# Kernel tuning notes

Measured on AMD Instinct MI355X. Metric: run time of the kernel, lower is better.

The kernel has to match this reference:

```python
import jax, jax.numpy as jnp
import numpy as np

K = 3            # kernel size (odd)
CO, CI = 16, 16  # out/in channels

def setup_inputs() -> dict:
    key = jax.random.key(0)
    k1, k2, k3, k4 = jax.random.split(key, 4)
    B, C, H, W = 4, CI, 128, 128
    input_data = jax.random.normal(k1, (B, C, H, W), dtype=jnp.float32)
    # fixation coordinates in pixel units
    foa_xy = jax.random.uniform(k2, (B, 2), dtype=jnp.float32) * jnp.array([W, H], jnp.float32)
    hidden = 256
    W1 = jax.random.normal(k3, (2, hidden), dtype=jnp.float32) * (1.0 / jnp.sqrt(2.0))
    b1 = jnp.zeros((hidden,), jnp.float32)
    W2 = jax.random.normal(k4, (hidden, CO * CI * K * K), dtype=jnp.float32) * (1.0 / jnp.sqrt(hidden))
    b2 = jnp.zeros((CO * CI * K * K,), jnp.float32)
    return {"input_data": input_data, "foa_xy": foa_xy, "W1": W1, "b1": b1, "W2": W2, "b2": b2}

def _unfold_reflect(x, k):
    # x: [B, C, H, W] -> patches [B, C, k*k, H*W], reflect padding, stride 1, dilation 1
    B, C, H, W = x.shape
    pad = (k - 1) // 2
    xp = jnp.pad(x, ((0, 0), (0, 0), (pad, pad), (pad, pad)), mode="reflect")
    rows = [xp[:, :, i:i + H, j:j + W] for i in range(k) for j in range(k)]
    return jnp.stack(rows, axis=2).reshape(B, C, k * k, H * W)

def reference(input_data, foa_xy, W1, b1, W2, b2):
    B, C, H, W = input_data.shape
    # coordinate grid [H*W, 2] as (x, y), matching torch meshgrid(ij) + stack(xx, yy)
    ys = jnp.arange(H, dtype=jnp.float32)
    xs = jnp.arange(W, dtype=jnp.float32)
    yy, xx = jnp.meshgrid(ys, xs, indexing="ij")
    coords = jnp.stack([xx.ravel(), yy.ravel()], axis=1)         # [HW, 2]
    net_in = (coords[None, :, :] - foa_xy[:, None, :]).reshape(B * H * W, 2)
    # kernel-generating MLP
    h = jax.nn.relu(net_in @ W1 + b1)
    net_out = h @ W2 + b2                                        # [B*HW, CO*CI*K*K]
    kernel = net_out.reshape(B, H * W, CO, CI, K * K)            # [B, P, o, i, q]
    patches = _unfold_reflect(input_data, K)                     # [B, CI, K*K, HW]
    # per-pixel conv: sum over in-channels and kernel taps
    out = jnp.einsum("biqp,bpoiq->bop", patches, kernel)         # [B, CO, HW]
    return out.reshape(B, CO, H, W)
```

## Files before the change

kernel.cpp:

```cpp
#include <hip/hip_runtime.h>

#define CI    16
#define CO    16
#define HID   256
#define KPAD  288
#define NKK   9
#define NKH   8
#define NCH   144
#define IMGH  128
#define IMGW  128
#define PTS   68
#define KKSTR (NCH * 32)
#define OSTRS (NKK * NCH * 32)

typedef float f32x4  __attribute__((ext_vector_type(4)));
typedef float f32x2  __attribute__((ext_vector_type(2)));
typedef short bf16x8 __attribute__((ext_vector_type(8)));

__device__ __host__ __forceinline__ short f2bf(float f) {
  union { float f; unsigned u; } c; c.f = f;
  unsigned b = c.u + 0x7FFFu + ((c.u >> 16) & 1u);
  return (short)(b >> 16);
}

__global__ void prep_w2(const float* __restrict__ W2, const float* __restrict__ b2,
                        short* __restrict__ W2b) {
  __shared__ float tile[32][65];
  const int kk = blockIdx.x % NKK;
  const int colbase = (blockIdx.x / NKK) * 64;
  const int tid = threadIdx.x;

  for (int e = tid; e < 2048; e += 256) {
    int klr = e >> 6;
    int cc  = e & 63;
    int col = colbase + cc;
    float v;
    if (kk < 8) v = W2[(kk * 32 + klr) * (CO * NCH) + col];
    else        v = (klr == 0) ? b2[col] : 0.f;
    tile[klr][cc] = v;
  }
  __syncthreads();
  for (int e = tid; e < 2048; e += 256) {
    int cc = e >> 5;
    int kl = e & 31;
    int col = colbase + cc;
    int o = col / NCH;
    int n = col - o * NCH;
    W2b[(((o * NKK + kk) * NCH + n) << 5) + kl] = f2bf(tile[kl][cc]);
  }
}

__global__ __launch_bounds__(256, 3)
void ngconv_main(const float* __restrict__ in, const float* __restrict__ foa,
                 const float* __restrict__ W1, const float* __restrict__ b1,
                 const short* __restrict__ W2b, float* __restrict__ out) {
  __shared__ short shHf[32 * 512];
  __shared__ short shPatchT[NCH * PTS];

  const int tid  = threadIdx.x;
  const int lane = tid & 63;
  const int wv   = tid >> 6;
  const int c15  = lane & 15;
  const int quad = lane >> 4;

  const int blk = blockIdx.x;
  const int b   = blk >> 8;
  const int rem = blk & 255;
  const int y   = rem >> 1;
  const int x0  = (rem & 1) << 6;

  const float fx  = foa[b * 2 + 0];
  const float fy  = foa[b * 2 + 1];
  const float dyv = (float)y - fy;

  const int ry0 = (y == 0) ? 1 : (y - 1);
  const int ry2 = (y == IMGH - 1) ? (IMGH - 2) : (y + 1);

  for (int e = tid; e < NCH * 64; e += 256) {
    int n  = e >> 6;
    int px = e & 63;
    int i = n / 9, q = n - i * 9;
    int dyr = q / 3, dx = q - dyr * 3;
    int ryr = (dyr == 0) ? ry0 : ((dyr == 1) ? y : ry2);
    int x = x0 + px + dx - 1;
    x = (x < 0) ? 1 : ((x > IMGW - 1) ? (IMGW - 2) : x);
    shPatchT[n * PTS + px] = f2bf(in[((b * CI + i) * IMGH + ryr) * IMGW + x]);
  }

  for (int g = tid; g < 64 * 32; g += 256) {
    int px = g & 63;
    int ks = g >> 6;
    int k0 = ks << 3;
    float dxv = (float)(x0 + px) - fx;
    short hv[8];
    #pragma unroll
    for (int j = 0; j < 8; ++j) {
      int k = k0 + j;
      float h = fmaxf(fmaf(dxv, W1[k], fmaf(dyv, W1[HID + k], b1[k])), 0.f);
      hv[j] = f2bf(h);
    }
    int ms = px >> 4;
    int kk = k0 >> 5;
    int lslot = ((k0 & 31) >> 3) * 16 + (px & 15);
    *(bf16x8*)&shHf[((ms * NKH + kk) << 9) + (lslot << 3)] = *(bf16x8*)hv;
  }

  bf16x8 af8 = (bf16x8){0, 0, 0, 0, 0, 0, 0, 0};
  if (quad == 0) af8[0] = (short)0x3F80;

  __syncthreads();

  #pragma unroll 1
  for (int oj = 0; oj < 4; ++oj) {
    const int o = wv + oj * 4;
    const short* Bo = W2b + o * OSTRS + (c15 << 5) + (quad << 3);

    f32x2 P2[8];
    #pragma unroll
    for (int t = 0; t < 8; ++t) P2[t] = (f32x2){0.f, 0.f};

    #pragma unroll 1
    for (int pass = 0; pass < 3; ++pass) {
      const short* Bp = Bo + (pass * 3) * 512;
      f32x4 acc[4][3];
      #pragma unroll
      for (int ms = 0; ms < 4; ++ms)
        #pragma unroll
        for (int j = 0; j < 3; ++j)
          acc[ms][j] = (f32x4){0.f, 0.f, 0.f, 0.f};

      bf16x8 bE[3], bO[3];
      #pragma unroll
      for (int j = 0; j < 3; ++j) bE[j] = *(const bf16x8*)&Bp[j << 9];

      #pragma unroll 1
      for (int t = 0; t < 4; ++t) {
        const int kkE = 2 * t;
        #pragma unroll
        for (int j = 0; j < 3; ++j)
          bO[j] = *(const bf16x8*)&Bp[(kkE + 1) * KKSTR + (j << 9)];
        {
          const short* hp = shHf + (kkE << 9) + (lane << 3);
          #pragma unroll
          for (int ms = 0; ms < 4; ++ms) {
            bf16x8 af = *(const bf16x8*)&hp[ms * (NKH << 9)];
            #pragma unroll
            for (int j = 0; j < 3; ++j)
              acc[ms][j] = __builtin_amdgcn_mfma_f32_16x16x32_bf16(
                  af, bE[j], acc[ms][j], 0, 0, 0);
          }
        }
        #pragma unroll
        for (int j = 0; j < 3; ++j)
          bE[j] = *(const bf16x8*)&Bp[(kkE + 2) * KKSTR + (j << 9)];
        {
          const short* hp = shHf + ((kkE + 1) << 9) + (lane << 3);
          #pragma unroll
          for (int ms = 0; ms < 4; ++ms) {
            bf16x8 af = *(const bf16x8*)&hp[ms * (NKH << 9)];
            #pragma unroll
            for (int j = 0; j < 3; ++j)
              acc[ms][j] = __builtin_amdgcn_mfma_f32_16x16x32_bf16(
                  af, bO[j], acc[ms][j], 0, 0, 0);
          }
        }
      }
      {
        #pragma unroll
        for (int ms = 0; ms < 4; ++ms)
          #pragma unroll
          for (int j = 0; j < 3; ++j)
            acc[ms][j] = __builtin_amdgcn_mfma_f32_16x16x32_bf16(
                af8, bE[j], acc[ms][j], 0, 0, 0);
      }

      #pragma unroll
      for (int j = 0; j < 3; ++j) {
        int n15 = ((pass * 3 + j) << 4) + c15;
        const short* prow = &shPatchT[n15 * PTS + (quad << 2)];
        #pragma unroll
        for (int ms = 0; ms < 4; ++ms) {
          uint2 u = *(const uint2*)&prow[ms * 16];
          float p0 = __uint_as_float(u.x << 16);
          float p1 = __uint_as_float(u.x & 0xFFFF0000u);
          float p2 = __uint_as_float(u.y << 16);
          float p3 = __uint_as_float(u.y & 0xFFFF0000u);
          f32x2 a01 = {acc[ms][j][0], acc[ms][j][1]};
          f32x2 a23 = {acc[ms][j][2], acc[ms][j][3]};
          P2[ms * 2 + 0] += a01 * (f32x2){p0, p1};
          P2[ms * 2 + 1] += a23 * (f32x2){p2, p3};
        }
      }
    }

    float P[16];
    #pragma unroll
    for (int t = 0; t < 16; ++t) P[t] = P2[t >> 1][t & 1];
    #pragma unroll
    for (int m = 8; m >= 1; m >>= 1) {
      const bool hi = (c15 & m) != 0;
      #pragma unroll
      for (int j = 0; j < m; ++j) {
        float keep = hi ? P[j + m] : P[j];
        float send = hi ? P[j] : P[j + m];
        float recv = __shfl_xor(send, m, 64);
        P[j] = keep + recv;
      }
    }

    const int x = x0 + (c15 >> 2) * 16 + quad * 4 + (c15 & 3);
    out[((b * CO + o) * IMGH + y) * IMGW + x] = P[0];
  }
}

extern "C" void kernel_launch(void* const* d_in, const int* in_sizes, int n_in,
                              void* d_out, int out_size, void* d_ws, size_t ws_size,
                              hipStream_t stream) {
  const float* in  = (const float*)d_in[0];
  const float* foa = (const float*)d_in[1];
  const float* W1  = (const float*)d_in[2];
  const float* b1  = (const float*)d_in[3];
  const float* W2  = (const float*)d_in[4];
  const float* b2  = (const float*)d_in[5];
  float* out = (float*)d_out;
  short* W2b = (short*)d_ws;

  prep_w2<<<324, 256, 0, stream>>>(W2, b2, W2b);
  ngconv_main<<<1024, 256, 0, stream>>>(in, foa, W1, b1, W2b, out);
}
```

Baseline: 184.2 us.

## Reorder patch channels by dx so shared patch buffer stores rows once

```diff
diff --git a/kernel.cpp b/kernel.cpp
--- a/kernel.cpp
+++ b/kernel.cpp
@@ -9,7 +9,7 @@
 #define NCH   144
 #define IMGH  128
 #define IMGW  128
-#define PTS   68
+#define RSTR  68
 #define KKSTR (NCH * 32)
 #define OSTRS (NKK * NCH * 32)
 
@@ -46,16 +46,19 @@
     int col = colbase + cc;
     int o = col / NCH;
     int n = col - o * NCH;
-    W2b[(((o * NKK + kk) * NCH + n) << 5) + kl] = f2bf(tile[kl][cc]);
-  }
-}
-
-__global__ __launch_bounds__(256, 3)
+    int i = n / 9, q = n - i * 9;
+    int dyr = q / 3, dx = q - dyr * 3;
+    int np = dx * 48 + i * 3 + dyr;
+    W2b[(((o * NKK + kk) * NCH + np) << 5) + kl] = f2bf(tile[kl][cc]);
+  }
+}
+
+__global__ __launch_bounds__(256, 4)
 void ngconv_main(const float* __restrict__ in, const float* __restrict__ foa,
                  const float* __restrict__ W1, const float* __restrict__ b1,
                  const short* __restrict__ W2b, float* __restrict__ out) {
   __shared__ short shHf[32 * 512];
-  __shared__ short shPatchT[NCH * PTS];
+  __shared__ short shPatch[48 * RSTR];
 
   const int tid  = threadIdx.x;
   const int lane = tid & 63;
@@ -76,15 +79,14 @@
   const int ry0 = (y == 0) ? 1 : (y - 1);
   const int ry2 = (y == IMGH - 1) ? (IMGH - 2) : (y + 1);
 
-  for (int e = tid; e < NCH * 64; e += 256) {
-    int n  = e >> 6;
-    int px = e & 63;
-    int i = n / 9, q = n - i * 9;
-    int dyr = q / 3, dx = q - dyr * 3;
+  for (int e = tid; e < 48 * 66; e += 256) {
+    int r  = e / 66;
+    int xx = e - r * 66;
+    int i = r / 3, dyr = r - i * 3;
     int ryr = (dyr == 0) ? ry0 : ((dyr == 1) ? y : ry2);
-    int x = x0 + px + dx - 1;
+    int x = x0 + xx - 1;
     x = (x < 0) ? 1 : ((x > IMGW - 1) ? (IMGW - 2) : x);
-    shPatchT[n * PTS + px] = f2bf(in[((b * CI + i) * IMGH + ryr) * IMGW + x]);
+    shPatch[r * RSTR + xx] = f2bf(in[((b * CI + i) * IMGH + ryr) * IMGW + x]);
   }
 
   for (int g = tid; g < 64 * 32; g += 256) {
@@ -174,17 +176,24 @@
                 af8, bE[j], acc[ms][j], 0, 0, 0);
       }
 
+      const int sh = pass << 4;
       #pragma unroll
       for (int j = 0; j < 3; ++j) {
-        int n15 = ((pass * 3 + j) << 4) + c15;
-        const short* prow = &shPatchT[n15 * PTS + (quad << 2)];
+        const short* prow = &shPatch[((j << 4) + c15) * RSTR + (quad << 2)];
         #pragma unroll
         for (int ms = 0; ms < 4; ++ms) {
-          uint2 u = *(const uint2*)&prow[ms * 16];
-          float p0 = __uint_as_float(u.x << 16);
-          float p1 = __uint_as_float(u.x & 0xFFFF0000u);
-          float p2 = __uint_as_float(u.y << 16);
-          float p3 = __uint_as_float(u.y & 0xFFFF0000u);
+          uint2 u0 = *(const uint2*)&prow[ms * 16];
+          unsigned u1 = *(const unsigned*)&prow[ms * 16 + 4];
+          unsigned long long a0 =
+              (unsigned long long)u0.x | ((unsigned long long)u0.y << 32);
+          unsigned long long a1 =
+              (unsigned long long)u0.y | ((unsigned long long)u1 << 32);
+          unsigned d0 = (unsigned)(a0 >> sh);
+          unsigned d1 = (unsigned)(a1 >> sh);
+          float p0 = __uint_as_float(d0 << 16);
+          float p1 = __uint_as_float(d0 & 0xFFFF0000u);
+          float p2 = __uint_as_float(d1 << 16);
+          float p3 = __uint_as_float(d1 & 0xFFFF0000u);
           f32x2 a01 = {acc[ms][j][0], acc[ms][j][1]};
           f32x2 a23 = {acc[ms][j][2], acc[ms][j][3]};
           P2[ms * 2 + 0] += a01 * (f32x2){p0, p1};
```

Result: slower. 189.9 us (+3.1%).
